# Kernel optimization log

Measured on AMD Instinct MI355X. Metric: run time of the kernel, lower is better.

Reference implementation:

```python
import jax, jax.numpy as jnp
import numpy as np

HEADS = 8
DIM_HEAD = 64
EPS = 1e-4
SCALE = DIM_HEAD ** -0.5


def setup_inputs() -> dict:
    key = jax.random.key(0)
    k1, k2, k3, k4 = jax.random.split(key, 4)
    dim = HEADS * DIM_HEAD  # 512
    x = jax.random.normal(k1, (2, 2048, dim), dtype=jnp.float32)
    # torch Linear weights are [out, in]; scale like default init
    Wq = jax.random.normal(k2, (dim, dim), dtype=jnp.float32) / np.sqrt(dim)
    Wkv = jax.random.normal(k3, (2 * dim, dim), dtype=jnp.float32) / np.sqrt(dim)
    Wout = jax.random.normal(k4, (dim, dim), dtype=jnp.float32) / np.sqrt(dim)
    return {"x": x, "Wq": Wq, "Wkv": Wkv, "Wout": Wout}


def _normalize_magnitude(t, eps=EPS):
    # divide by (sqrt(mean(t^2, -1)) + eps)
    mag = jnp.sqrt(jnp.mean(t * t, axis=-1, keepdims=True)) + eps
    return t / mag


def reference(x, Wq, Wkv, Wout):
    b, n, dim = x.shape
    h, d = HEADS, DIM_HEAD
    # norm=False -> Identity; context = x (self-attention)
    q = x @ Wq.T                      # [b, n, h*d]
    kv = x @ Wkv.T                    # [b, n, 2*h*d]
    k, v = jnp.split(kv, 2, axis=-1)
    def to_heads(t):
        return t.reshape(b, n, h, d).transpose(0, 2, 1, 3)  # [b, h, n, d]
    q, k, v = map(to_heads, (q, k, v))
    q = _normalize_magnitude(q)
    k = _normalize_magnitude(k)
    sim = jnp.einsum('bhid,bhjd->bhij', q, k) * SCALE
    attn = jax.nn.softmax(sim, axis=-1)
    out = jnp.einsum('bhij,bhjd->bhid', attn, v)
    out = out.transpose(0, 2, 1, 3).reshape(b, n, h * d)
    return out @ Wout.T
```

## Files before the change

### kernel.cpp

```cpp
#include <hip/hip_runtime.h>

typedef __bf16 bf16x8 __attribute__((ext_vector_type(8)));
typedef __bf16 bf16x4 __attribute__((ext_vector_type(4)));
typedef float  f32x4  __attribute__((ext_vector_type(4)));

#define LOG2E_F 1.44269504088896340736f

static constexpr int kB = 2, kN = 2048, kH = 8, kD = 64, kDim = 512;
static constexpr int kTok = kB * kN;
static constexpr int kNQKV = 1536;
static constexpr int kKH = 3;

__device__ __forceinline__ void gld16(const void* g, void* l) {
  __builtin_amdgcn_global_load_lds(
      (const __attribute__((address_space(1))) void*)g,
      (__attribute__((address_space(3))) void*)l, 16, 0, 0);
}


__global__ __launch_bounds__(256) void cvt_all(const float* __restrict__ x,
                                               const float* __restrict__ wq,
                                               const float* __restrict__ wkv,
                                               const float* __restrict__ wo,
                                               __bf16* __restrict__ xb,
                                               __bf16* __restrict__ wqkvb,
                                               __bf16* __restrict__ wob) {
  size_t i = ((size_t)blockIdx.x * 256 + threadIdx.x) * 8;
  const float* s; __bf16* d; size_t off;
  if (i < 2097152)      { s = x;   d = xb;              off = i; }
  else if (i < 2359296) { s = wq;  d = wqkvb;           off = i - 2097152; }
  else if (i < 2883584) { s = wkv; d = wqkvb + 262144;  off = i - 2359296; }
  else                  { s = wo;  d = wob;             off = i - 2883584; }
  float4 u = *(const float4*)(s + off);
  float4 v = *(const float4*)(s + off + 4);
  bf16x8 t;
  t[0] = (__bf16)u.x; t[1] = (__bf16)u.y; t[2] = (__bf16)u.z; t[3] = (__bf16)u.w;
  t[4] = (__bf16)v.x; t[5] = (__bf16)v.y; t[6] = (__bf16)v.z; t[7] = (__bf16)v.w;
  *(bf16x8*)(d + off) = t;
}

__global__ __launch_bounds__(256, 3) void gemm_qkv(const __bf16* __restrict__ A,
                                                   const __bf16* __restrict__ B,
                                                   __bf16* __restrict__ qn,
                                                   __bf16* __restrict__ kn,
                                                   __bf16* __restrict__ vt2) {
  const int K = kDim;
  const int tid = threadIdx.x;
  const int w = tid >> 6, lane = tid & 63, quad = lane >> 4, lq = lane & 15;
  const int m0 = blockIdx.y * 128;
  const int n0 = blockIdx.x * 64;
  const int wm = w * 32;
  __shared__ __bf16 As[2][128 * 64];
  __shared__ __bf16 Bs[2][64 * 64];

  const f32x4 zero = {0.f, 0.f, 0.f, 0.f};
  f32x4 acc[2][4];
#pragma unroll
  for (int fm = 0; fm < 2; ++fm)
#pragma unroll
    for (int fn = 0; fn < 4; ++fn) acc[fm][fn] = zero;

  const int sr = tid >> 3, ch = tid & 7;
  auto stage = [&](int k0, int buf) {
#pragma unroll
    for (int j = 0; j < 4; ++j) {
      const int row = j * 32 + sr;
      gld16(A + (size_t)(m0 + row) * K + k0 + ((ch ^ (row & 7)) << 3),
            &As[buf][row * 64 + ch * 8]);
    }
#pragma unroll
    for (int j = 0; j < 2; ++j) {
      const int row = j * 32 + sr;
      gld16(B + (size_t)(n0 + row) * K + k0 + ((ch ^ (row & 7)) << 3),
            &Bs[buf][row * 64 + ch * 8]);
    }
  };
  const int sw0 = ((quad ^ (lq & 7)) << 3);
  const int sw1 = (((4 | quad) ^ (lq & 7)) << 3);

  stage(0, 0);
  for (int i = 0; i < 8; ++i) {
    __syncthreads();
    if (i + 1 < 8) stage((i + 1) << 6, (i + 1) & 1);
    const __bf16* as = As[i & 1];
    const __bf16* bs = Bs[i & 1];
#pragma unroll
    for (int ks = 0; ks < 2; ++ks) {
      const int sw = ks ? sw1 : sw0;
      bf16x8 a[2], b[4];
#pragma unroll
      for (int fm = 0; fm < 2; ++fm)
        a[fm] = *(const bf16x8*)&as[(wm + fm * 16 + lq) * 64 + sw];
#pragma unroll
      for (int fn = 0; fn < 4; ++fn)
        b[fn] = *(const bf16x8*)&bs[(fn * 16 + lq) * 64 + sw];
#pragma unroll
      for (int fm = 0; fm < 2; ++fm)
#pragma unroll
        for (int fn = 0; fn < 4; ++fn)
          acc[fm][fn] =
              __builtin_amdgcn_mfma_f32_16x16x32_bf16(a[fm], b[fn], acc[fm][fn], 0, 0, 0);
    }
  }

  const int h = (n0 >> 6) & 7;
  if (n0 >= 1024) {
    __syncthreads();
    __bf16* Ts = &As[0][0];
#pragma unroll
    for (int fm = 0; fm < 2; ++fm)
#pragma unroll
      for (int r = 0; r < 4; ++r) {
        const int mo = wm + fm * 16 + quad * 4 + r;
        const int tau = mo >> 6, tt = mo & 63;
        const int p = (tt & 15) * 4 + (tt >> 4);
#pragma unroll
        for (int fn = 0; fn < 4; ++fn)
          Ts[tau * 4608 + (fn * 16 + lq) * 72 + p] = (__bf16)acc[fm][fn][r];
      }
    __syncthreads();
    const int b = m0 >> 11, kt0 = (m0 & (kN - 1)) >> 6;
    const int dd = tid >> 2, p0 = (tid & 3) << 4;
#pragma unroll
    for (int tau = 0; tau < 2; ++tau) {
      const __bf16* src = Ts + tau * 4608 + dd * 72 + p0;
      __bf16* dst = vt2 + ((size_t)((b * kH + h) * 32 + kt0 + tau)) * 4096 + tid * 16;
      *(bf16x8*)dst = *(const bf16x8*)src;
      *(bf16x8*)(dst + 8) = *(const bf16x8*)(src + 8);
    }
  } else {
    const float qs = (n0 < 512) ? (0.125f * LOG2E_F) : 1.0f;
    __bf16* dst0 = (n0 < 512) ? qn : kn;
#pragma unroll
    for (int fm = 0; fm < 2; ++fm)
#pragma unroll
      for (int r = 0; r < 4; ++r) {
        float ss = 0.f;
#pragma unroll
        for (int fn = 0; fn < 4; ++fn) ss += acc[fm][fn][r] * acc[fm][fn][r];
#pragma unroll
        for (int off = 1; off < 16; off <<= 1) ss += __shfl_xor(ss, off, 64);
        const float inv = qs / (sqrtf(ss * (1.f / 64)) + 1e-4f);
        const int m = m0 + wm + fm * 16 + quad * 4 + r;
        const int b = m >> 11, n = m & (kN - 1);
        __bf16* dst = dst0 + ((size_t)(b * kH + h) * kN + n) * kD;
#pragma unroll
        for (int fn = 0; fn < 4; ++fn)
          dst[fn * 16 + lq] = (__bf16)(acc[fm][fn][r] * inv);
      }
  }
}

__global__ __launch_bounds__(256, 3) void attn(const __bf16* __restrict__ qn,
                                               const __bf16* __restrict__ kn,
                                               const __bf16* __restrict__ vt2,
                                               __bf16* __restrict__ po,
                                               float* __restrict__ pl) {
  const int qt = blockIdx.x, bh = blockIdx.y, kh = blockIdx.z;
  const int kt0 = kh * 11;
  const int cnt = (kh == 2) ? 10 : 11;
  const int tid = threadIdx.x;
  const int w = tid >> 6, lane = tid & 63, quad = lane >> 4, lq = lane & 15;
  __shared__ __bf16 Ks[2][4096];
  __shared__ __bf16 Vs[2][4096];
  __shared__ __bf16 Ps[4][32 * 72];
  __bf16* myP = Ps[w];

  bf16x8 aq[2][2];
#pragma unroll
  for (int fm = 0; fm < 2; ++fm) {
    const __bf16* Qb = qn + ((size_t)bh * kN + qt * 128 + w * 32 + fm * 16 + lq) * kD;
    aq[fm][0] = *(const bf16x8*)(Qb + quad * 8);
    aq[fm][1] = *(const bf16x8*)(Qb + 32 + quad * 8);
  }

  const f32x4 zero  = {0.f, 0.f, 0.f, 0.f};
  const f32x4 minit = {-12.f, -12.f, -12.f, -12.f};
  f32x4 o[2][4];
  float lr[2][4];
#pragma unroll
  for (int fm = 0; fm < 2; ++fm)
#pragma unroll
    for (int i = 0; i < 4; ++i) { o[fm][i] = zero; lr[fm][i] = 0.f; }

  const __bf16* Kb = kn + (size_t)bh * kN * kD;
  const __bf16* Vb = vt2 + (size_t)bh * 32 * 4096;

  auto stage = [&](int ktg, int buf) {
#pragma unroll
    for (int j = 0; j < 2; ++j) {
      const int s = j * 256 + tid;
      const int row = s >> 3, ch = s & 7;
      const int src = row * 64 + ((ch ^ (row & 7)) << 3);
      gld16(Kb + (size_t)ktg * 4096 + src, &Ks[buf][s * 8]);
      gld16(Vb + (size_t)ktg * 4096 + src, &Vs[buf][s * 8]);
    }
  };
  const int sw0 = ((quad ^ (lq & 7)) << 3);
  const int sw1 = (((4 | quad) ^ (lq & 7)) << 3);

  stage(kt0, 0);
  for (int kt = 0; kt < cnt; ++kt) {
    __syncthreads();
    if (kt + 1 < cnt) stage(kt0 + kt + 1, (kt + 1) & 1);
    const __bf16* ks_ = Ks[kt & 1];
    const __bf16* vs_ = Vs[kt & 1];

    bf16x8 kb0[4], kb1[4], vb0[4], vb1[4];
#pragma unroll
    for (int fn = 0; fn < 4; ++fn) {
      const int rb = (fn * 16 + lq) * 64;
      kb0[fn] = *(const bf16x8*)&ks_[rb + sw0];
      kb1[fn] = *(const bf16x8*)&ks_[rb + sw1];
      vb0[fn] = *(const bf16x8*)&vs_[rb + sw0];
      vb1[fn] = *(const bf16x8*)&vs_[rb + sw1];
    }
    f32x4 s[2][4];
#pragma unroll
    for (int fm = 0; fm < 2; ++fm)
#pragma unroll
      for (int fn = 0; fn < 4; ++fn) {
        f32x4 a = __builtin_amdgcn_mfma_f32_16x16x32_bf16(aq[fm][0], kb0[fn], minit, 0, 0, 0);
        s[fm][fn] = __builtin_amdgcn_mfma_f32_16x16x32_bf16(aq[fm][1], kb1[fn], a, 0, 0, 0);
      }

#pragma unroll
    for (int fm = 0; fm < 2; ++fm)
#pragma unroll
      for (int r = 0; r < 4; ++r) {
        const float p0 = __builtin_amdgcn_exp2f(s[fm][0][r]);
        const float p1 = __builtin_amdgcn_exp2f(s[fm][1][r]);
        const float p2 = __builtin_amdgcn_exp2f(s[fm][2][r]);
        const float p3 = __builtin_amdgcn_exp2f(s[fm][3][r]);
        lr[fm][r] += (p0 + p1) + (p2 + p3);
        bf16x4 pk = {(__bf16)p0, (__bf16)p1, (__bf16)p2, (__bf16)p3};
        *(bf16x4*)&myP[(fm * 16 + quad * 4 + r) * 72 + lq * 4] = pk;
      }

#pragma unroll
    for (int fm = 0; fm < 2; ++fm) {
      bf16x8 ap0 = *(const bf16x8*)&myP[(fm * 16 + lq) * 72 + quad * 8];
      bf16x8 ap1 = *(const bf16x8*)&myP[(fm * 16 + lq) * 72 + 32 + quad * 8];
#pragma unroll
      for (int fn = 0; fn < 4; ++fn) {
        o[fm][fn] = __builtin_amdgcn_mfma_f32_16x16x32_bf16(ap0, vb0[fn], o[fm][fn], 0, 0, 0);
        o[fm][fn] = __builtin_amdgcn_mfma_f32_16x16x32_bf16(ap1, vb1[fn], o[fm][fn], 0, 0, 0);
      }
    }
  }

  const int b = bh >> 3, h = bh & 7;
#pragma unroll
  for (int fm = 0; fm < 2; ++fm) {
    const int qrow0 = qt * 128 + w * 32 + fm * 16 + quad * 4;
#pragma unroll
    for (int r = 0; r < 4; ++r) {
      float sum = lr[fm][r];
#pragma unroll
      for (int off = 1; off < 16; off <<= 1) sum += __shfl_xor(sum, off, 64);
      if (lq == 0) pl[(size_t)kh * 32768 + bh * kN + qrow0 + r] = sum;
      const size_t ob = ((size_t)kh * kTok + b * kN + qrow0 + r) * kDim + h * 64;
#pragma unroll
      for (int fn = 0; fn < 4; ++fn) po[ob + fn * 16 + lq] = (__bf16)o[fm][fn][r];
    }
  }
}

__global__ __launch_bounds__(256) void combine(const __bf16* __restrict__ po,
                                               const float* __restrict__ pl,
                                               __bf16* __restrict__ ao) {
  const size_t i = ((size_t)blockIdx.x * 256 + threadIdx.x) * 4;
  const int tok = (int)(i >> 9), dk = (int)(i & 511);
  const int h = dk >> 6, b = tok >> 11, qrow = tok & (kN - 1);
  const int idx = (b * kH + h) * kN + qrow;
  float l = 0.f;
#pragma unroll
  for (int kh = 0; kh < kKH; ++kh) l += pl[kh * 32768 + idx];
  const float inv = 1.f / l;
  float s0 = 0.f, s1 = 0.f, s2 = 0.f, s3 = 0.f;
#pragma unroll
  for (int kh = 0; kh < kKH; ++kh) {
    bf16x4 a = *(const bf16x4*)(po + (size_t)kh * kTok * kDim + i);
    s0 += (float)a[0]; s1 += (float)a[1]; s2 += (float)a[2]; s3 += (float)a[3];
  }
  bf16x4 t = {(__bf16)(s0 * inv), (__bf16)(s1 * inv),
              (__bf16)(s2 * inv), (__bf16)(s3 * inv)};
  *(bf16x4*)(ao + i) = t;
}

__global__ __launch_bounds__(256, 2) void gemm64(const __bf16* __restrict__ A,
                                                 const __bf16* __restrict__ B,
                                                 float* __restrict__ C,
                                                 int N, int K) {
  const int tid = threadIdx.x;
  const int w = tid >> 6, lane = tid & 63, quad = lane >> 4, lq = lane & 15;
  const int m0 = blockIdx.y * 64;
  const int n0 = blockIdx.x * 64;
  const int wm = (w >> 1) * 32, wn = (w & 1) * 32;
  __shared__ __bf16 As[2][4096];
  __shared__ __bf16 Bs[2][4096];

  const f32x4 zero = {0.f, 0.f, 0.f, 0.f};
  f32x4 acc00 = zero, acc01 = zero, acc10 = zero, acc11 = zero;

  const int sr = tid >> 3, ch = tid & 7;
  auto stage = [&](int k0, int buf) {
#pragma unroll
    for (int j = 0; j < 2; ++j) {
      const int row = j * 32 + sr;
      const int src = k0 + ((ch ^ (row & 7)) << 3);
      gld16(A + (size_t)(m0 + row) * K + src, &As[buf][row * 64 + ch * 8]);
      gld16(B + (size_t)(n0 + row) * K + src, &Bs[buf][row * 64 + ch * 8]);
    }
  };
  const int sw0 = ((quad ^ (lq & 7)) << 3);
  const int sw1 = (((4 | quad) ^ (lq & 7)) << 3);

  stage(0, 0);
  const int iters = K >> 6;
  for (int i = 0; i < iters; ++i) {
    __syncthreads();
    if (i + 1 < iters) stage((i + 1) << 6, (i + 1) & 1);
    const __bf16* as = As[i & 1];
    const __bf16* bs = Bs[i & 1];
#pragma unroll
    for (int ks = 0; ks < 2; ++ks) {
      const int sw = ks ? sw1 : sw0;
      bf16x8 a0 = *(const bf16x8*)&as[(wm +      lq) * 64 + sw];
      bf16x8 a1 = *(const bf16x8*)&as[(wm + 16 + lq) * 64 + sw];
      bf16x8 b0 = *(const bf16x8*)&bs[(wn +      lq) * 64 + sw];
      bf16x8 b1 = *(const bf16x8*)&bs[(wn + 16 + lq) * 64 + sw];
      acc00 = __builtin_amdgcn_mfma_f32_16x16x32_bf16(a0, b0, acc00, 0, 0, 0);
      acc01 = __builtin_amdgcn_mfma_f32_16x16x32_bf16(a0, b1, acc01, 0, 0, 0);
      acc10 = __builtin_amdgcn_mfma_f32_16x16x32_bf16(a1, b0, acc10, 0, 0, 0);
      acc11 = __builtin_amdgcn_mfma_f32_16x16x32_bf16(a1, b1, acc11, 0, 0, 0);
    }
  }
  const f32x4 av[2][2] = {{acc00, acc01}, {acc10, acc11}};
#pragma unroll
  for (int fm = 0; fm < 2; ++fm)
#pragma unroll
    for (int fn = 0; fn < 2; ++fn)
#pragma unroll
      for (int r = 0; r < 4; ++r)
        C[(size_t)(m0 + wm + fm * 16 + quad * 4 + r) * N + (n0 + wn + fn * 16 + lq)] =
            av[fm][fn][r];
}

extern "C" void kernel_launch(void* const* d_in, const int* in_sizes, int n_in,
                              void* d_out, int out_size, void* d_ws, size_t ws_size,
                              hipStream_t stream) {
  const float* x    = (const float*)d_in[0];
  const float* Wq   = (const float*)d_in[1];
  const float* Wkv  = (const float*)d_in[2];
  const float* Wout = (const float*)d_in[3];
  float* out = (float*)d_out;
  char* ws = (char*)d_ws;

  __bf16* xb    = (__bf16*)(ws);
  __bf16* wqkvb = (__bf16*)(ws + (size_t)(4 << 20));
  __bf16* wob   = (__bf16*)(ws + (size_t)(6 << 20));
  __bf16* qn    = (__bf16*)(ws + (size_t)(7 << 20));
  __bf16* kn    = (__bf16*)(ws + (size_t)(11 << 20));
  __bf16* vt2   = (__bf16*)(ws + (size_t)(15 << 20));
  __bf16* po    = (__bf16*)(ws + (size_t)(19 << 20));
  float*  pl    = (float*)(ws + (size_t)(32 << 20));
  __bf16* ao    = (__bf16*)(ws + (size_t)(33 << 20));

  cvt_all<<<1536, 256, 0, stream>>>(x, Wq, Wkv, Wout, xb, wqkvb, wob);
  gemm_qkv<<<dim3(kNQKV / 64, kTok / 128), 256, 0, stream>>>(xb, wqkvb, qn, kn, vt2);
  attn<<<dim3(kN / 128, kB * kH, kKH), 256, 0, stream>>>(qn, kn, vt2, po, pl);
  combine<<<kTok * kDim / 1024, 256, 0, stream>>>(po, pl, ao);
  gemm64<<<dim3(kDim / 64, kTok / 64), 256, 0, stream>>>(ao, wob, out, kDim, kDim);
}
```

Measured before the change: 118.2 us.

## Compute S transposed and reshuffle P via permlane swaps instead of LDS

The QK^T MFMA now uses swapped operands, producing S^T so that each lane holds values for a single query row. The probabilities are packed to bf16 and redistributed into the PV A-operand layout with permlane16/permlane32 swaps, removing the per-wave LDS staging buffer and its write/read round trip. Row sums become per-lane and need only two cross-quad shuffles. The key split also goes from 3 to 4 chunks of 8 tiles with occupancy hint 4, and the workspace is rearranged so the partial outputs fit (ao now reuses the xb region).

```diff
diff --git a/kernel.cpp b/kernel.cpp
--- a/kernel.cpp
+++ b/kernel.cpp
@@ -2,19 +2,27 @@
 
 typedef __bf16 bf16x8 __attribute__((ext_vector_type(8)));
 typedef __bf16 bf16x4 __attribute__((ext_vector_type(4)));
+typedef __bf16 bf16x2 __attribute__((ext_vector_type(2)));
 typedef float  f32x4  __attribute__((ext_vector_type(4)));
+typedef unsigned int u32x2 __attribute__((ext_vector_type(2)));
+typedef unsigned int u32x4 __attribute__((ext_vector_type(4)));
 
 #define LOG2E_F 1.44269504088896340736f
 
 static constexpr int kB = 2, kN = 2048, kH = 8, kD = 64, kDim = 512;
 static constexpr int kTok = kB * kN;
 static constexpr int kNQKV = 1536;
-static constexpr int kKH = 3;
+static constexpr int kKH = 4;
 
 __device__ __forceinline__ void gld16(const void* g, void* l) {
   __builtin_amdgcn_global_load_lds(
       (const __attribute__((address_space(1))) void*)g,
       (__attribute__((address_space(3))) void*)l, 16, 0, 0);
+}
+
+__device__ __forceinline__ unsigned pkbf(float a, float b) {
+  bf16x2 v; v[0] = (__bf16)a; v[1] = (__bf16)b;
+  return __builtin_bit_cast(unsigned, v);
 }
 
 
@@ -151,20 +159,17 @@
   }
 }
 
-__global__ __launch_bounds__(256, 3) void attn(const __bf16* __restrict__ qn,
+__global__ __launch_bounds__(256, 4) void attn(const __bf16* __restrict__ qn,
                                                const __bf16* __restrict__ kn,
                                                const __bf16* __restrict__ vt2,
                                                __bf16* __restrict__ po,
                                                float* __restrict__ pl) {
   const int qt = blockIdx.x, bh = blockIdx.y, kh = blockIdx.z;
-  const int kt0 = kh * 11;
-  const int cnt = (kh == 2) ? 10 : 11;
+  const int kt0 = kh * 8, cnt = 8;
   const int tid = threadIdx.x;
   const int w = tid >> 6, lane = tid & 63, quad = lane >> 4, lq = lane & 15;
   __shared__ __bf16 Ks[2][4096];
   __shared__ __bf16 Vs[2][4096];
-  __shared__ __bf16 Ps[4][32 * 72];
-  __bf16* myP = Ps[w];
 
   bf16x8 aq[2][2];
 #pragma unroll
@@ -177,11 +182,11 @@
   const f32x4 zero  = {0.f, 0.f, 0.f, 0.f};
   const f32x4 minit = {-12.f, -12.f, -12.f, -12.f};
   f32x4 o[2][4];
-  float lr[2][4];
+  float lr[2] = {0.f, 0.f};
 #pragma unroll
   for (int fm = 0; fm < 2; ++fm)
 #pragma unroll
-    for (int i = 0; i < 4; ++i) { o[fm][i] = zero; lr[fm][i] = 0.f; }
+    for (int i = 0; i < 4; ++i) o[fm][i] = zero;
 
   const __bf16* Kb = kn + (size_t)bh * kN * kD;
   const __bf16* Vb = vt2 + (size_t)bh * 32 * 4096;
@@ -206,60 +211,80 @@
     const __bf16* ks_ = Ks[kt & 1];
     const __bf16* vs_ = Vs[kt & 1];
 
-    bf16x8 kb0[4], kb1[4], vb0[4], vb1[4];
+    bf16x8 kb0[4], kb1[4];
 #pragma unroll
     for (int fn = 0; fn < 4; ++fn) {
       const int rb = (fn * 16 + lq) * 64;
       kb0[fn] = *(const bf16x8*)&ks_[rb + sw0];
       kb1[fn] = *(const bf16x8*)&ks_[rb + sw1];
+    }
+
+    bf16x8 pa[2][2];
+#pragma unroll
+    for (int fm = 0; fm < 2; ++fm) {
+      f32x4 s[4];
+#pragma unroll
+      for (int fn = 0; fn < 4; ++fn) {
+        f32x4 a = __builtin_amdgcn_mfma_f32_16x16x32_bf16(kb0[fn], aq[fm][0], minit, 0, 0, 0);
+        s[fn] = __builtin_amdgcn_mfma_f32_16x16x32_bf16(kb1[fn], aq[fm][1], a, 0, 0, 0);
+      }
+      float p[4][4];
+      float ls = 0.f;
+#pragma unroll
+      for (int fn = 0; fn < 4; ++fn)
+#pragma unroll
+        for (int r = 0; r < 4; ++r) {
+          p[fn][r] = __builtin_amdgcn_exp2f(s[fn][r]);
+          ls += p[fn][r];
+        }
+      lr[fm] += ls;
+      unsigned Wp[2][4];
+#pragma unroll
+      for (int j = 0; j < 2; ++j)
+#pragma unroll
+        for (int r = 0; r < 4; ++r) Wp[j][r] = pkbf(p[2 * j][r], p[2 * j + 1][r]);
+      unsigned pw[2][4];
+#pragma unroll
+      for (int wi = 0; wi < 4; ++wi) {
+        const int j = wi & 1, dl = wi >> 1;
+        u32x2 t1 = __builtin_amdgcn_permlane16_swap(Wp[j][dl], Wp[j][2 + dl], false, false);
+        u32x2 t2 = __builtin_amdgcn_permlane32_swap(t1[0], t1[1], false, false);
+        pw[0][wi] = t2[0]; pw[1][wi] = t2[1];
+      }
+#pragma unroll
+      for (int ks = 0; ks < 2; ++ks) {
+        u32x4 pv = {pw[ks][0], pw[ks][1], pw[ks][2], pw[ks][3]};
+        pa[fm][ks] = __builtin_bit_cast(bf16x8, pv);
+      }
+    }
+
+    bf16x8 vb0[4], vb1[4];
+#pragma unroll
+    for (int fn = 0; fn < 4; ++fn) {
+      const int rb = (fn * 16 + lq) * 64;
       vb0[fn] = *(const bf16x8*)&vs_[rb + sw0];
       vb1[fn] = *(const bf16x8*)&vs_[rb + sw1];
     }
-    f32x4 s[2][4];
 #pragma unroll
     for (int fm = 0; fm < 2; ++fm)
 #pragma unroll
       for (int fn = 0; fn < 4; ++fn) {
-        f32x4 a = __builtin_amdgcn_mfma_f32_16x16x32_bf16(aq[fm][0], kb0[fn], minit, 0, 0, 0);
-        s[fm][fn] = __builtin_amdgcn_mfma_f32_16x16x32_bf16(aq[fm][1], kb1[fn], a, 0, 0, 0);
-      }
-
-#pragma unroll
-    for (int fm = 0; fm < 2; ++fm)
-#pragma unroll
-      for (int r = 0; r < 4; ++r) {
-        const float p0 = __builtin_amdgcn_exp2f(s[fm][0][r]);
-        const float p1 = __builtin_amdgcn_exp2f(s[fm][1][r]);
-        const float p2 = __builtin_amdgcn_exp2f(s[fm][2][r]);
-        const float p3 = __builtin_amdgcn_exp2f(s[fm][3][r]);
-        lr[fm][r] += (p0 + p1) + (p2 + p3);
-        bf16x4 pk = {(__bf16)p0, (__bf16)p1, (__bf16)p2, (__bf16)p3};
-        *(bf16x4*)&myP[(fm * 16 + quad * 4 + r) * 72 + lq * 4] = pk;
-      }
-
-#pragma unroll
-    for (int fm = 0; fm < 2; ++fm) {
-      bf16x8 ap0 = *(const bf16x8*)&myP[(fm * 16 + lq) * 72 + quad * 8];
-      bf16x8 ap1 = *(const bf16x8*)&myP[(fm * 16 + lq) * 72 + 32 + quad * 8];
-#pragma unroll
-      for (int fn = 0; fn < 4; ++fn) {
-        o[fm][fn] = __builtin_amdgcn_mfma_f32_16x16x32_bf16(ap0, vb0[fn], o[fm][fn], 0, 0, 0);
-        o[fm][fn] = __builtin_amdgcn_mfma_f32_16x16x32_bf16(ap1, vb1[fn], o[fm][fn], 0, 0, 0);
-      }
-    }
+        o[fm][fn] = __builtin_amdgcn_mfma_f32_16x16x32_bf16(pa[fm][0], vb0[fn], o[fm][fn], 0, 0, 0);
+        o[fm][fn] = __builtin_amdgcn_mfma_f32_16x16x32_bf16(pa[fm][1], vb1[fn], o[fm][fn], 0, 0, 0);
+      }
   }
 
   const int b = bh >> 3, h = bh & 7;
 #pragma unroll
   for (int fm = 0; fm < 2; ++fm) {
-    const int qrow0 = qt * 128 + w * 32 + fm * 16 + quad * 4;
+    float sum = lr[fm];
+    sum += __shfl_xor(sum, 16, 64);
+    sum += __shfl_xor(sum, 32, 64);
+    const int qbase = qt * 128 + w * 32 + fm * 16;
+    if (quad == 0) pl[(size_t)kh * 32768 + bh * kN + qbase + lq] = sum;
 #pragma unroll
     for (int r = 0; r < 4; ++r) {
-      float sum = lr[fm][r];
-#pragma unroll
-      for (int off = 1; off < 16; off <<= 1) sum += __shfl_xor(sum, off, 64);
-      if (lq == 0) pl[(size_t)kh * 32768 + bh * kN + qrow0 + r] = sum;
-      const size_t ob = ((size_t)kh * kTok + b * kN + qrow0 + r) * kDim + h * 64;
+      const size_t ob = ((size_t)kh * kTok + b * kN + qbase + quad * 4 + r) * kDim + h * 64;
 #pragma unroll
       for (int fn = 0; fn < 4; ++fn) po[ob + fn * 16 + lq] = (__bf16)o[fm][fn][r];
     }
@@ -364,8 +389,8 @@
   __bf16* kn    = (__bf16*)(ws + (size_t)(11 << 20));
   __bf16* vt2   = (__bf16*)(ws + (size_t)(15 << 20));
   __bf16* po    = (__bf16*)(ws + (size_t)(19 << 20));
-  float*  pl    = (float*)(ws + (size_t)(32 << 20));
-  __bf16* ao    = (__bf16*)(ws + (size_t)(33 << 20));
+  float*  pl    = (float*)(ws + (size_t)(35 << 20));
+  __bf16* ao    = (__bf16*)(ws);
 
   cvt_all<<<1536, 256, 0, stream>>>(x, Wq, Wkv, Wout, xb, wqkvb, wob);
   gemm_qkv<<<dim3(kNQKV / 64, kTok / 128), 256, 0, stream>>>(xb, wqkvb, qn, kn, vt2);
```

Result: slower. 124.4 us (+5.2%).
